# Kernel optimization log

Hardware: AMD Instinct MI355X
Metric: run time of the kernel (lower is better)

The kernel has to match this reference:

```python
import jax, jax.numpy as jnp
import numpy as np

B, L, HID = 2, 2048, 1024
H = 16
D = HID // H          # head_dim = 64
LR = 16               # gate low-rank dim
EPS = 1e-5
GLN = 16.0            # gate_logit_normalizer
SCALE = D ** -0.5


def setup_inputs() -> dict:
    key = jax.random.key(0)
    ks = jax.random.split(key, 9)
    s = 0.02
    return {
        "x": jax.random.normal(ks[0], (B, L, HID), jnp.float32),
        "Wq": jax.random.normal(ks[1], (HID, HID), jnp.float32) * s,
        "Wk": jax.random.normal(ks[2], (HID, HID), jnp.float32) * s,
        "Wv": jax.random.normal(ks[3], (HID, HID), jnp.float32) * s,
        "Wg1": jax.random.normal(ks[4], (HID, LR), jnp.float32) * s,
        "Wg2": jax.random.normal(ks[5], (LR, HID), jnp.float32) * s,
        "bg2": jnp.zeros((HID,), jnp.float32),
        "Wg": jax.random.normal(ks[6], (HID, HID), jnp.float32) * s,
        "g_norm_w": jnp.ones((D,), jnp.float32),
        "Wo": jax.random.normal(ks[7], (HID, HID), jnp.float32) * s,
    }


def reference(x, Wq, Wk, Wv, Wg1, Wg2, bg2, Wg, g_norm_w, Wo):
    Bb, Ll, Hid = x.shape
    q = (x @ Wq).reshape(Bb, Ll, H, D)
    k = (x @ Wk).reshape(Bb, Ll, H, D)
    v = (x @ Wv).reshape(Bb, Ll, H, D)
    gk = jax.nn.log_sigmoid(((x @ Wg1) @ Wg2 + bg2)).reshape(Bb, Ll, H, D) / GLN

    def step(S, inp):
        q_t, k_t, v_t, gk_t = inp  # each (B, H, D)
        # S: (B,H,D,D); gate broadcasts over the v-dim (last axis)
        S = jnp.exp(gk_t)[..., None] * S + k_t[..., None] * v_t[..., None, :]
        o_t = jnp.einsum('bhdv,bhd->bhv', S, q_t) * SCALE  # S^T @ q / sqrt(D)
        return S, o_t

    S0 = jnp.zeros((Bb, H, D, D), x.dtype)
    scan_in = tuple(jnp.moveaxis(t, 1, 0) for t in (q, k, v, gk))  # (L,B,H,D)
    S, o = jax.lax.scan(step, S0, scan_in)
    o = jnp.moveaxis(o, 0, 1)  # (B, L, H, D)

    # RMSNorm over head_dim with affine weight
    o = o * jax.lax.rsqrt(jnp.mean(o * o, axis=-1, keepdims=True) + EPS) * g_norm_w
    o = o.reshape(Bb, Ll, Hid)

    # Swish output gate
    g = x @ Wg
    o = o * (g * jax.nn.sigmoid(g))
    o = o @ Wo
    return o, S[:, None]  # last_state: (B,1,H,D,D)
```

## Files before the change

### kernel.cpp

```cpp
#include <hip/hip_runtime.h>
#include <hip/hip_bf16.h>

typedef unsigned short u16;
typedef __attribute__((ext_vector_type(8))) short bf16x8;
typedef __attribute__((ext_vector_type(4))) float f32x4;

#define L_SEQ 2048
#define HID 1024
#define NC 32
#define MTOK 4096
#define GEPS 1e-5f
#define QSCALE 0.125f

__device__ __forceinline__ float bf2f(u16 u){ union{unsigned i; float f;}c; c.i=(unsigned)u<<16; return c.f; }
__device__ __forceinline__ u16 f2bf(float f){ union{__hip_bfloat16 h; u16 u;}c; c.h=__float2bfloat16(f); return c.u; }

__device__ __forceinline__ int swz72(int row, int col){ return row * 72 + (col ^ ((row >> 1) & 24)); }
__device__ __forceinline__ int swzc(int t){ return ((t >> 2) & 3) << 3; }

__device__ __forceinline__ void gload_lds16(const u16* g, u16* l){
  __builtin_amdgcn_global_load_lds((const __attribute__((address_space(1))) void*)g,
                                   (__attribute__((address_space(3))) void*)l, 16, 0, 0);
}

__global__ __launch_bounds__(256) void gla_prep(const float* __restrict__ x,
                                                u16* __restrict__ xb,
                                                const float* W0, const float* W1,
                                                const float* W2, const float* W3,
                                                const float* W4,
                                                u16* D0, u16* D1, u16* D2, u16* D3, u16* D4){
  __shared__ float tile[32][33];
  int bid = blockIdx.x;
  if (bid < 2048){
    size_t i = ((size_t)bid * 256 + threadIdx.x) * 8;
    float4 a = *(const float4*)&x[i];
    float4 b = *(const float4*)&x[i + 4];
    u16 o[8] __attribute__((aligned(16))) = {
      f2bf(a.x), f2bf(a.y), f2bf(a.z), f2bf(a.w),
      f2bf(b.x), f2bf(b.y), f2bf(b.z), f2bf(b.w) };
    *(uint4*)&xb[i] = *(uint4*)o;
  } else {
    int id = bid - 2048;
    int z = id >> 10, rem = id & 1023;
    int bx = rem & 31, by = rem >> 5;
    const float* W; u16* D;
    switch (z){
      case 0: W = W0; D = D0; break;
      case 1: W = W1; D = D1; break;
      case 2: W = W2; D = D2; break;
      case 3: W = W3; D = D3; break;
      default: W = W4; D = D4; break;
    }
    int tx = threadIdx.x & 31, ty = threadIdx.x >> 5;
    int n0 = bx * 32, k0 = by * 32;
    #pragma unroll
    for (int r = ty; r < 32; r += 8)
      tile[r][tx] = W[(size_t)(k0 + r) * HID + n0 + tx];
    __syncthreads();
    #pragma unroll
    for (int r = ty; r < 32; r += 8)
      D[(size_t)(n0 + r) * HID + k0 + tx] = f2bf(tile[tx][r]);
  }
}

__global__ __launch_bounds__(256) void gla_xg1_mfma(const u16* __restrict__ xb,
                                                    const float* __restrict__ Wg1,
                                                    float* __restrict__ xg1){
  __shared__ u16 WL[16 * 1032];
  #pragma unroll 8
  for (int i = 0; i < 64; i++){
    int flat = i * 256 + threadIdx.x;
    int k = flat >> 4, n = flat & 15;
    WL[n * 1032 + k] = f2bf(Wg1[flat]);
  }
  __syncthreads();
  int lane = threadIdx.x & 63, w = threadIdx.x >> 6;
  int lr = lane & 15, lk = lane >> 4;
  int rt = blockIdx.x * 4 + w;
  const u16* Arow = xb + ((size_t)rt * 16 + lr) * HID;
  f32x4 acc;
  #pragma unroll
  for (int e = 0; e < 4; e++) acc[e] = 0.f;
  #pragma unroll 4
  for (int ks = 0; ks < 32; ks++){
    bf16x8 a = *(const bf16x8*)&Arow[ks * 32 + lk * 8];
    bf16x8 b = *(const bf16x8*)&WL[lr * 1032 + ks * 32 + lk * 8];
    acc = __builtin_amdgcn_mfma_f32_16x16x32_bf16(a, b, acc, 0, 0, 0);
  }
  #pragma unroll
  for (int r = 0; r < 4; r++)
    xg1[(size_t)(rt * 16 + lk * 4 + r) * 16 + lr] = acc[r];
}

__global__ __launch_bounds__(256) void gla_gkcg(const float* __restrict__ xg1,
                                                const float* __restrict__ Wg2,
                                                const float* __restrict__ bg2,
                                                u16* __restrict__ CG){
  __shared__ float xs[64][16];
  int blk = blockIdx.x;
  int b = blk >> 7, r7 = blk & 127;
  int c = r7 >> 2, q = r7 & 3;
  int col = q * 256 + threadIdx.x;
  int tok0 = b * L_SEQ + c * 64;
  {
    int row = threadIdx.x >> 2, e4 = (threadIdx.x & 3) * 4;
    *(float4*)&xs[row][e4] = *(const float4*)&xg1[(size_t)(tok0 + row) * 16 + e4];
  }
  __syncthreads();
  float w[16];
  #pragma unroll
  for (int r = 0; r < 16; r++) w[r] = Wg2[r * HID + col];
  float bz = bg2[col];
  float cum = 0.f;
  for (int t = 0; t < 64; t++){
    float z = bz;
    #pragma unroll
    for (int r = 0; r < 16; r++) z += xs[t][r] * w[r];
    float ls = -__logf(1.f + __expf(-z));
    cum += ls * (1.0f / 16.0f);
    CG[(size_t)(tok0 + t) * HID + col] = f2bf(cum);
  }
}

__global__ __launch_bounds__(512) void gla_gemm_qkvg(const u16* __restrict__ A,
                                                     const u16* __restrict__ Bt,
                                                     u16* __restrict__ C){
  constexpr int NT = HID / 32;
  __shared__ u16 As[2][256 * 32];
  __shared__ u16 Bs[2][128 * 32];
  const int tid = threadIdx.x;
  const int lane = tid & 63, wid = tid >> 6;
  const int wm = wid >> 1, wn = wid & 1;
  const int lr = lane & 15, lk = lane >> 4;
  const int id = blockIdx.x + 16 * blockIdx.y;
  const int nid = (id & 7) * 64 + (id >> 3);
  const int bm = nid & 15, bn = nid >> 4;
  const int srow = tid >> 2;
  const int skw  = ((tid & 3) * 8) ^ ((srow & 3) << 3);
  const u16* Ag = A  + ((size_t)bm * 256 + srow) * HID + skw;
  const u16* Bg = Bt + ((size_t)bn * 128 + srow) * HID + skw;

  f32x4 acc[4][4];
  #pragma unroll
  for (int i = 0; i < 4; i++)
    #pragma unroll
    for (int j = 0; j < 4; j++)
      #pragma unroll
      for (int e = 0; e < 4; e++) acc[i][j][e] = 0.f;

  auto STAGE = [&](int buf, int kt){
    gload_lds16(Ag + kt * 32,                         &As[buf][tid * 8]);
    gload_lds16(Ag + (size_t)128 * HID + kt * 32,     &As[buf][4096 + tid * 8]);
    gload_lds16(Bg + kt * 32,                         &Bs[buf][tid * 8]);
  };

  STAGE(0, 0);
  for (int t = 0; t < NT; ++t){
    const int buf = t & 1;
    if (t + 1 < NT){
      STAGE(buf ^ 1, t + 1);
      asm volatile("s_waitcnt vmcnt(3)\ns_barrier" ::: "memory");
    } else {
      asm volatile("s_waitcnt vmcnt(0)\ns_barrier" ::: "memory");
    }
    bf16x8 af[4], bfr[4];
    #pragma unroll
    for (int m = 0; m < 4; m++){
      int row = wm * 64 + m * 16 + lr;
      af[m] = *(const bf16x8*)&As[buf][(row * 32 + lk * 8) ^ ((row & 3) << 3)];
    }
    #pragma unroll
    for (int n = 0; n < 4; n++){
      int row = wn * 64 + n * 16 + lr;
      bfr[n] = *(const bf16x8*)&Bs[buf][(row * 32 + lk * 8) ^ ((row & 3) << 3)];
    }
    __builtin_amdgcn_s_setprio(1);
    #pragma unroll
    for (int m = 0; m < 4; m++)
      #pragma unroll
      for (int n = 0; n < 4; n++)
        acc[m][n] = __builtin_amdgcn_mfma_f32_16x16x32_bf16(af[m], bfr[n], acc[m][n], 0, 0, 0);
    __builtin_amdgcn_s_setprio(0);
    __builtin_amdgcn_sched_barrier(0);
    asm volatile("s_barrier" ::: "memory");
  }

  #pragma unroll
  for (int i = 0; i < 4; i++)
    #pragma unroll
    for (int j = 0; j < 4; j++){
      int row0 = bm * 256 + wm * 64 + i * 16 + lk * 4;
      int cb   = bn * 128 + wn * 64 + j * 16 + lr;
      int sel  = cb >> 10, col = cb & 1023;
      size_t base = (size_t)sel * ((size_t)MTOK * HID) + (size_t)row0 * HID + col;
      #pragma unroll
      for (int r = 0; r < 4; r++)
        C[base + (size_t)r * HID] = f2bf(acc[i][j][r]);
    }
}

__global__ __launch_bounds__(256) void gla_gemm_out2(const u16* __restrict__ A,
                                                     const u16* __restrict__ Bt,
                                                     float* __restrict__ C){
  constexpr int NT = 16;
  __shared__ __align__(16) char smem[49152];
  const int tid = threadIdx.x;
  const int lane = tid & 63, wid = tid >> 6;
  const int kg = wid >> 1, w = wid & 1;
  const int lr = lane & 15, lk = lane >> 4;
  const int bm = blockIdx.x, bn = blockIdx.y;
  const int srow = tid >> 2;
  const int skw  = ((tid & 3) * 8) ^ ((srow & 3) << 3);
  const u16* Ag = A  + ((size_t)bm * 64  + srow) * HID + skw;
  const u16* Bg = Bt + ((size_t)bn * 128 + srow) * HID + skw;
  auto seg = [&](int g, int buf) -> u16* { return (u16*)(smem + (g * 2 + buf) * 12288); };

  f32x4 acc[4][4];
  #pragma unroll
  for (int i = 0; i < 4; i++)
    #pragma unroll
    for (int j = 0; j < 4; j++)
      #pragma unroll
      for (int e = 0; e < 4; e++) acc[i][j][e] = 0.f;

  auto STAGE = [&](int buf, int kt){
    gload_lds16(Ag + kt * 32,                          seg(0, buf) + tid * 8);
    gload_lds16(Bg + kt * 32,                          seg(0, buf) + 2048 + tid * 8);
    gload_lds16(Bg + (size_t)64 * HID + kt * 32,       seg(0, buf) + 4096 + tid * 8);
    gload_lds16(Ag + 512 + kt * 32,                    seg(1, buf) + tid * 8);
    gload_lds16(Bg + 512 + kt * 32,                    seg(1, buf) + 2048 + tid * 8);
    gload_lds16(Bg + (size_t)64 * HID + 512 + kt * 32, seg(1, buf) + 4096 + tid * 8);
  };

  STAGE(0, 0);
  for (int t = 0; t < NT; ++t){
    const int buf = t & 1;
    if (t + 1 < NT){
      STAGE(buf ^ 1, t + 1);
      asm volatile("s_waitcnt vmcnt(6)\ns_barrier" ::: "memory");
    } else {
      asm volatile("s_waitcnt vmcnt(0)\ns_barrier" ::: "memory");
    }
    const u16* Ab = seg(kg, buf);
    const u16* Bb = seg(kg, buf) + 2048;
    bf16x8 af[4], bfr[4];
    #pragma unroll
    for (int m = 0; m < 4; m++){
      int row = m * 16 + lr;
      af[m] = *(const bf16x8*)&Ab[(row * 32 + lk * 8) ^ ((row & 3) << 3)];
    }
    #pragma unroll
    for (int n = 0; n < 4; n++){
      int row = w * 64 + n * 16 + lr;
      bfr[n] = *(const bf16x8*)&Bb[(row * 32 + lk * 8) ^ ((row & 3) << 3)];
    }
    __builtin_amdgcn_s_setprio(1);
    #pragma unroll
    for (int m = 0; m < 4; m++)
      #pragma unroll
      for (int n = 0; n < 4; n++)
        acc[m][n] = __builtin_amdgcn_mfma_f32_16x16x32_bf16(af[m], bfr[n], acc[m][n], 0, 0, 0);
    __builtin_amdgcn_s_setprio(0);
    __builtin_amdgcn_sched_barrier(0);
    asm volatile("s_barrier" ::: "memory");
  }

  float* red = (float*)smem;
  if (kg == 1){
    #pragma unroll
    for (int m = 0; m < 4; m++)
      #pragma unroll
      for (int n = 0; n < 4; n++){
        int lrow = m * 16 + lk * 4, lcol = w * 64 + n * 16 + lr;
        #pragma unroll
        for (int r = 0; r < 4; r++)
          red[(lrow + r) * 132 + lcol] = acc[m][n][r];
      }
  }
  __syncthreads();
  if (kg == 0){
    #pragma unroll
    for (int m = 0; m < 4; m++)
      #pragma unroll
      for (int n = 0; n < 4; n++){
        int lrow = m * 16 + lk * 4, lcol = w * 64 + n * 16 + lr;
        #pragma unroll
        for (int r = 0; r < 4; r++)
          C[(size_t)(bm * 64 + lrow + r) * HID + bn * 128 + lcol] =
              acc[m][n][r] + red[(lrow + r) * 132 + lcol];
      }
  }
}

__global__ __launch_bounds__(256) void gla_chunk_state2(const u16* __restrict__ Kb,
                                                        const u16* __restrict__ Vb,
                                                        const u16* __restrict__ CG,
                                                        u16* __restrict__ Tbuf,
                                                        float* __restrict__ Dbuf){
  __shared__ u16 KHT[64 * 72];
  __shared__ u16 VT[64 * 72];
  int blk = blockIdx.x;
  int c = blk & (NC - 1), bh = blk >> 5;
  int b = bh >> 4, h = bh & 15;
  int tid = threadIdx.x;
  int lane = tid & 63, w = tid >> 6;
  int lr = lane & 15, lk = lane >> 4;
  int tr = tid >> 2, tc = (tid & 3) * 16;
  size_t gbase = ((size_t)(b * L_SEQ + c * 64)) * HID + h * 64;

  float cg[16], cgl[16];
  {
    const u16* cgp = CG + gbase + (size_t)tr * HID + tc;
    const u16* clp = CG + gbase + (size_t)63 * HID + tc;
    uint4 a0 = *(const uint4*)cgp, a1 = *(const uint4*)(cgp + 8);
    uint4 l0 = *(const uint4*)clp, l1 = *(const uint4*)(clp + 8);
    const u16* au = (const u16*)&a0; const u16* au2 = (const u16*)&a1;
    const u16* lu = (const u16*)&l0; const u16* lu2 = (const u16*)&l1;
    #pragma unroll
    for (int e = 0; e < 8; e++){
      cg[e] = bf2f(au[e]); cg[8 + e] = bf2f(au2[e]);
      cgl[e] = bf2f(lu[e]); cgl[8 + e] = bf2f(lu2[e]);
    }
  }
  {
    const u16* kp = Kb + gbase + (size_t)tr * HID + tc;
    const u16* vp = Vb + gbase + (size_t)tr * HID + tc;
    uint4 kr0 = *(const uint4*)kp, kr1 = *(const uint4*)(kp + 8);
    uint4 vr0 = *(const uint4*)vp, vr1 = *(const uint4*)(vp + 8);
    const u16* ku = (const u16*)&kr0; const u16* ku2 = (const u16*)&kr1;
    const u16* vu = (const u16*)&vr0; const u16* vu2 = (const u16*)&vr1;
    #pragma unroll
    for (int e = 0; e < 8; e++){
      KHT[swz72(tc + e, tr)]     = f2bf(bf2f(ku[e])  * __expf(cgl[e]     - cg[e]));
      KHT[swz72(tc + 8 + e, tr)] = f2bf(bf2f(ku2[e]) * __expf(cgl[8 + e] - cg[8 + e]));
      VT[swz72(tc + e, tr)]      = vu[e];
      VT[swz72(tc + 8 + e, tr)]  = vu2[e];
    }
  }
  if (tr == 0){
    #pragma unroll
    for (int e = 0; e < 16; e++)
      Dbuf[(size_t)blk * 64 + tc + e] = __expf(cgl[e]);
  }
  __syncthreads();
  int R0 = w * 16;
  f32x4 tacc[4];
  #pragma unroll
  for (int v = 0; v < 4; v++)
    #pragma unroll
    for (int e = 0; e < 4; e++) tacc[v][e] = 0.f;
  #pragma unroll
  for (int ks = 0; ks < 2; ks++){
    bf16x8 a = *(const bf16x8*)&KHT[swz72(R0 + lr, ks * 32 + lk * 8)];
    #pragma unroll
    for (int v0 = 0; v0 < 4; v0++){
      bf16x8 bb = *(const bf16x8*)&VT[swz72(v0 * 16 + lr, ks * 32 + lk * 8)];
      tacc[v0] = __builtin_amdgcn_mfma_f32_16x16x32_bf16(a, bb, tacc[v0], 0, 0, 0);
    }
  }
  u16* Tp = Tbuf + (size_t)blk * 4096;
  #pragma unroll
  for (int v0 = 0; v0 < 4; v0++){
    int d = R0 + lk * 4, v = v0 * 16 + lr;
    #pragma unroll
    for (int r = 0; r < 4; r++)
      Tp[(d + r) * 64 + v] = f2bf(tacc[v0][r]);
  }
}

__global__ __launch_bounds__(256) void gla_state_scan2(const u16* __restrict__ Tbuf,
                                                       const float* __restrict__ Dbuf,
                                                       float* __restrict__ Sfin,
                                                       u16* __restrict__ Sinb){
  int bh = blockIdx.x >> 4, seg = blockIdx.x & 15;
  int dv = seg * 256 + threadIdx.x;
  int d = dv >> 6;
  float S = 0.f;
  for (int c = 0; c < NC; c++){
    size_t slot = (size_t)bh * NC + c;
    float t  = bf2f(Tbuf[slot * 4096 + dv]);
    float dec = Dbuf[slot * 64 + d];
    Sinb[slot * 4096 + dv] = f2bf(S);
    S = dec * S + t;
  }
  Sfin[(size_t)bh * 4096 + dv] = S;
}

__global__ __launch_bounds__(256) void gla_chunk_out2(const u16* __restrict__ Qb,
                                                      const u16* __restrict__ Kb,
                                                      const u16* __restrict__ Vb,
                                                      const u16* __restrict__ CG,
                                                      const u16* __restrict__ Sinb,
                                                      const u16* __restrict__ Gb,
                                                      const float* __restrict__ gnw,
                                                      u16* __restrict__ OG){
  __shared__ u16 QT[64 * 72];
  __shared__ u16 KP[64 * 72];
  __shared__ u16 VT[64 * 72];
  __shared__ u16 ST[64 * 72];
  int blk = blockIdx.x;
  int c = blk & (NC - 1), bh = blk >> 5;
  int b = bh >> 4, h = bh & 15;
  int tid = threadIdx.x;
  int lane = tid & 63, w = tid >> 6;
  int lr = lane & 15, lk = lane >> 4;
  int tr = tid >> 2, tc = (tid & 3) * 16;
  size_t gbase = ((size_t)(b * L_SEQ + c * 64)) * HID + h * 64;

  {
    float cg[16];
    const u16* cgp = CG + gbase + (size_t)tr * HID + tc;
    uint4 a0 = *(const uint4*)cgp, a1 = *(const uint4*)(cgp + 8);
    const u16* au = (const u16*)&a0; const u16* au2 = (const u16*)&a1;
    #pragma unroll
    for (int e = 0; e < 8; e++){ cg[e] = bf2f(au[e]); cg[8 + e] = bf2f(au2[e]); }
    const u16* qp = Qb + gbase + (size_t)tr * HID + tc;
    const u16* kp = Kb + gbase + (size_t)tr * HID + tc;
    const u16* vp = Vb + gbase + (size_t)tr * HID + tc;
    uint4 qr0 = *(const uint4*)qp, qr1 = *(const uint4*)(qp + 8);
    uint4 kr0 = *(const uint4*)kp, kr1 = *(const uint4*)(kp + 8);
    uint4 vr0 = *(const uint4*)vp, vr1 = *(const uint4*)(vp + 8);
    const u16* qu = (const u16*)&qr0; const u16* qu2 = (const u16*)&qr1;
    const u16* ku = (const u16*)&kr0; const u16* ku2 = (const u16*)&kr1;
    const u16* vu = (const u16*)&vr0; const u16* vu2 = (const u16*)&vr1;
    u16 qt[16] __attribute__((aligned(16)));
    u16 kt[16] __attribute__((aligned(16)));
    #pragma unroll
    for (int e = 0; e < 8; e++){
      float ec0 = __expf(cg[e]),  ei0 = __expf(-cg[e]);
      float ec1 = __expf(cg[8+e]), ei1 = __expf(-cg[8+e]);
      qt[e]     = f2bf(bf2f(qu[e])  * ec0 * QSCALE);
      qt[8 + e] = f2bf(bf2f(qu2[e]) * ec1 * QSCALE);
      kt[e]     = f2bf(bf2f(ku[e])  * ei0);
      kt[8 + e] = f2bf(bf2f(ku2[e]) * ei1);
      VT[swz72(tc + e, tr)]     = vu[e];
      VT[swz72(tc + 8 + e, tr)] = vu2[e];
    }
    *(uint4*)&QT[tr * 72 + tc]     = *(uint4*)&qt[0];
    *(uint4*)&QT[tr * 72 + tc + 8] = *(uint4*)&qt[8];
    *(uint4*)&KP[tr * 72 + tc]     = *(uint4*)&kt[0];
    *(uint4*)&KP[tr * 72 + tc + 8] = *(uint4*)&kt[8];
    const u16* sp = Sinb + (size_t)blk * 4096 + (size_t)tr * 64 + tc;
    uint4 s0 = *(const uint4*)sp, s1 = *(const uint4*)(sp + 8);
    const u16* su = (const u16*)&s0; const u16* su2 = (const u16*)&s1;
    #pragma unroll
    for (int e = 0; e < 8; e++){
      ST[swz72(tc + e, tr)]     = su[e];
      ST[swz72(tc + 8 + e, tr)] = su2[e];
    }
  }
  __syncthreads();

  int R0 = w * 16;
  f32x4 pacc[4];
  #pragma unroll
  for (int j = 0; j < 4; j++)
    #pragma unroll
    for (int e = 0; e < 4; e++) pacc[j][e] = 0.f;
  #pragma unroll
  for (int ks = 0; ks < 2; ks++){
    bf16x8 a = *(const bf16x8*)&QT[(R0 + lr) * 72 + ks * 32 + lk * 8];
    #pragma unroll
    for (int j0 = 0; j0 < 4; j0++){
      bf16x8 bb = *(const bf16x8*)&KP[(j0 * 16 + lr) * 72 + ks * 32 + lk * 8];
      pacc[j0] = __builtin_amdgcn_mfma_f32_16x16x32_bf16(a, bb, pacc[j0], 0, 0, 0);
    }
  }
  __syncthreads();

  #pragma unroll
  for (int j0 = 0; j0 < 4; j0++){
    int j = j0 * 16 + lr;
    #pragma unroll
    for (int r = 0; r < 4; r++){
      int t = R0 + lk * 4 + r;
      KP[t * 72 + (j ^ swzc(t))] = (j <= t) ? f2bf(pacc[j0][r]) : (u16)0;
    }
  }

  f32x4 oacc[4];
  #pragma unroll
  for (int v = 0; v < 4; v++)
    #pragma unroll
    for (int e = 0; e < 4; e++) oacc[v][e] = 0.f;
  #pragma unroll
  for (int ks = 0; ks < 2; ks++){
    bf16x8 a = *(const bf16x8*)&QT[(R0 + lr) * 72 + ks * 32 + lk * 8];
    #pragma unroll
    for (int v0 = 0; v0 < 4; v0++){
      bf16x8 bb = *(const bf16x8*)&ST[swz72(v0 * 16 + lr, ks * 32 + lk * 8)];
      oacc[v0] = __builtin_amdgcn_mfma_f32_16x16x32_bf16(a, bb, oacc[v0], 0, 0, 0);
    }
  }
  #pragma unroll
  for (int ks = 0; ks < 2; ks++){
    int arow = R0 + lr;
    bf16x8 a = *(const bf16x8*)&KP[arow * 72 + ((ks * 32 + lk * 8) ^ swzc(arow))];
    #pragma unroll
    for (int v0 = 0; v0 < 4; v0++){
      bf16x8 bb = *(const bf16x8*)&VT[swz72(v0 * 16 + lr, ks * 32 + lk * 8)];
      oacc[v0] = __builtin_amdgcn_mfma_f32_16x16x32_bf16(a, bb, oacc[v0], 0, 0, 0);
    }
  }

  {
    float gv[4][4];
    #pragma unroll
    for (int r = 0; r < 4; r++){
      int t = R0 + lk * 4 + r;
      #pragma unroll
      for (int v0 = 0; v0 < 4; v0++)
        gv[r][v0] = bf2f(Gb[gbase + (size_t)t * HID + v0 * 16 + lr]);
    }
    float gnv[4];
    #pragma unroll
    for (int v0 = 0; v0 < 4; v0++) gnv[v0] = gnw[v0 * 16 + lr];
    #pragma unroll
    for (int r = 0; r < 4; r++){
      float ssq = 0.f;
      #pragma unroll
      for (int v0 = 0; v0 < 4; v0++) ssq += oacc[v0][r] * oacc[v0][r];
      ssq += __shfl_xor(ssq, 1, 64);
      ssq += __shfl_xor(ssq, 2, 64);
      ssq += __shfl_xor(ssq, 4, 64);
      ssq += __shfl_xor(ssq, 8, 64);
      float rn = rsqrtf(ssq * (1.0f / 64.0f) + GEPS);
      int t = R0 + lk * 4 + r;
      #pragma unroll
      for (int v0 = 0; v0 < 4; v0++){
        float g = gv[r][v0];
        float sw = g / (1.f + __expf(-g));
        QT[t * 72 + ((v0 * 16 + lr) ^ swzc(t))] = f2bf(oacc[v0][r] * rn * gnv[v0] * sw);
      }
    }
  }
  __syncthreads();
  {
    int x0 = swzc(tr);
    uint4 o0 = *(uint4*)&QT[tr * 72 + (tc ^ x0)];
    uint4 o1 = *(uint4*)&QT[tr * 72 + ((tc + 8) ^ x0)];
    u16* op = OG + gbase + (size_t)tr * HID + tc;
    *(uint4*)op       = o0;
    *(uint4*)(op + 8) = o1;
  }
}

extern "C" void kernel_launch(void* const* d_in, const int* in_sizes, int n_in,
                              void* d_out, int out_size, void* d_ws, size_t ws_size,
                              hipStream_t stream){
  (void)in_sizes; (void)n_in; (void)out_size;
  const float* x   = (const float*)d_in[0];
  const float* Wq  = (const float*)d_in[1];
  const float* Wk  = (const float*)d_in[2];
  const float* Wv  = (const float*)d_in[3];
  const float* Wg1 = (const float*)d_in[4];
  const float* Wg2 = (const float*)d_in[5];
  const float* bg2 = (const float*)d_in[6];
  const float* Wg  = (const float*)d_in[7];
  const float* gnw = (const float*)d_in[8];
  const float* Wo  = (const float*)d_in[9];
  float* out = (float*)d_out;

  char* ws = (char*)d_ws;
  size_t off = 0;
  auto alloc = [&](size_t bytes) -> char* {
    char* p = ws + off; off += (bytes + 255) & ~(size_t)255; return p;
  };
  u16* xb   = (u16*)alloc((size_t)MTOK * HID * 2);
  u16* WTq  = (u16*)alloc((size_t)HID * HID * 2);
  u16* WTk  = (u16*)alloc((size_t)HID * HID * 2);
  u16* WTv  = (u16*)alloc((size_t)HID * HID * 2);
  u16* WTg  = (u16*)alloc((size_t)HID * HID * 2);
  u16* WTo  = (u16*)alloc((size_t)HID * HID * 2);
  u16* Qb   = (u16*)alloc((size_t)MTOK * HID * 2);
  u16* Kb   = (u16*)alloc((size_t)MTOK * HID * 2);
  u16* Vb   = (u16*)alloc((size_t)MTOK * HID * 2);
  u16* Gb   = (u16*)alloc((size_t)MTOK * HID * 2);
  u16* CGb  = (u16*)alloc((size_t)MTOK * HID * 2);
  float* xg1b = (float*)alloc((size_t)MTOK * 16 * 4);
  u16* Tbuf = (u16*)alloc((size_t)1024 * 4096 * 2);
  float* Dbuf = (float*)alloc((size_t)1024 * 64 * 4);
  u16* Sinb = (u16*)alloc((size_t)1024 * 4096 * 2);
  u16* OG   = (u16*)alloc((size_t)MTOK * HID * 2);
  if (off > ws_size) return;

  gla_prep<<<7168, 256, 0, stream>>>(x, xb, Wq, Wk, Wv, Wg, Wo,
                                     WTq, WTk, WTv, WTg, WTo);
  gla_xg1_mfma<<<64, 256, 0, stream>>>(xb, Wg1, xg1b);
  gla_gkcg<<<256, 256, 0, stream>>>(xg1b, Wg2, bg2, CGb);

  dim3 gq(16, 32);
  gla_gemm_qkvg<<<gq, 512, 0, stream>>>(xb, WTq, Qb);

  gla_chunk_state2<<<1024, 256, 0, stream>>>(Kb, Vb, CGb, Tbuf, Dbuf);
  gla_state_scan2<<<512, 256, 0, stream>>>(Tbuf, Dbuf, out + (size_t)MTOK * HID, Sinb);
  gla_chunk_out2<<<1024, 256, 0, stream>>>(Qb, Kb, Vb, CGb, Sinb, Gb, gnw, OG);

  dim3 go(64, 8);
  gla_gemm_out2<<<go, 256, 0, stream>>>(OG, WTo, out);
}
```

Measured before the change: 118.6 us.

## Fold gate low-rank GEMM into prep, parallelize gate cumsum, vectorize state scan

The x@Wg1 MFMA kernel is merged into the prep kernel as extra blocks that read fp32 x directly and convert it to bf16 on the fly, which removes one launch. The gate cumsum kernel is rewritten to use 1024 blocks, each covering a 64-token by 64-column tile. The sigmoid values go through shared memory and a two-level prefix sum replaces the serial 64-step loop per thread. The state scan now handles two elements per thread with packed 32-bit loads and stores, using half as many blocks. Together these target launch overhead and the low parallelism of the serial gate scan, at the cost of more shared memory per block and more synchronization.

```diff
diff --git a/kernel.cpp b/kernel.cpp
--- a/kernel.cpp
+++ b/kernel.cpp
@@ -25,11 +25,13 @@
 
 __global__ __launch_bounds__(256) void gla_prep(const float* __restrict__ x,
                                                 u16* __restrict__ xb,
+                                                const float* __restrict__ Wg1,
+                                                float* __restrict__ xg1,
                                                 const float* W0, const float* W1,
                                                 const float* W2, const float* W3,
                                                 const float* W4,
                                                 u16* D0, u16* D1, u16* D2, u16* D3, u16* D4){
-  __shared__ float tile[32][33];
+  __shared__ union { float tile[32][33]; u16 WL[16 * 1032]; } sh;
   int bid = blockIdx.x;
   if (bid < 2048){
     size_t i = ((size_t)bid * 256 + threadIdx.x) * 8;
@@ -39,7 +41,7 @@
       f2bf(a.x), f2bf(a.y), f2bf(a.z), f2bf(a.w),
       f2bf(b.x), f2bf(b.y), f2bf(b.z), f2bf(b.w) };
     *(uint4*)&xb[i] = *(uint4*)o;
-  } else {
+  } else if (bid < 7168){
     int id = bid - 2048;
     int z = id >> 10, rem = id & 1023;
     int bx = rem & 31, by = rem >> 5;
@@ -55,71 +57,92 @@
     int n0 = bx * 32, k0 = by * 32;
     #pragma unroll
     for (int r = ty; r < 32; r += 8)
-      tile[r][tx] = W[(size_t)(k0 + r) * HID + n0 + tx];
+      sh.tile[r][tx] = W[(size_t)(k0 + r) * HID + n0 + tx];
     __syncthreads();
     #pragma unroll
     for (int r = ty; r < 32; r += 8)
-      D[(size_t)(n0 + r) * HID + k0 + tx] = f2bf(tile[tx][r]);
-  }
-}
-
-__global__ __launch_bounds__(256) void gla_xg1_mfma(const u16* __restrict__ xb,
-                                                    const float* __restrict__ Wg1,
-                                                    float* __restrict__ xg1){
-  __shared__ u16 WL[16 * 1032];
-  #pragma unroll 8
-  for (int i = 0; i < 64; i++){
-    int flat = i * 256 + threadIdx.x;
-    int k = flat >> 4, n = flat & 15;
-    WL[n * 1032 + k] = f2bf(Wg1[flat]);
-  }
-  __syncthreads();
-  int lane = threadIdx.x & 63, w = threadIdx.x >> 6;
-  int lr = lane & 15, lk = lane >> 4;
-  int rt = blockIdx.x * 4 + w;
-  const u16* Arow = xb + ((size_t)rt * 16 + lr) * HID;
-  f32x4 acc;
-  #pragma unroll
-  for (int e = 0; e < 4; e++) acc[e] = 0.f;
-  #pragma unroll 4
-  for (int ks = 0; ks < 32; ks++){
-    bf16x8 a = *(const bf16x8*)&Arow[ks * 32 + lk * 8];
-    bf16x8 b = *(const bf16x8*)&WL[lr * 1032 + ks * 32 + lk * 8];
-    acc = __builtin_amdgcn_mfma_f32_16x16x32_bf16(a, b, acc, 0, 0, 0);
-  }
-  #pragma unroll
-  for (int r = 0; r < 4; r++)
-    xg1[(size_t)(rt * 16 + lk * 4 + r) * 16 + lr] = acc[r];
-}
-
-__global__ __launch_bounds__(256) void gla_gkcg(const float* __restrict__ xg1,
-                                                const float* __restrict__ Wg2,
-                                                const float* __restrict__ bg2,
-                                                u16* __restrict__ CG){
-  __shared__ float xs[64][16];
+      D[(size_t)(n0 + r) * HID + k0 + tx] = f2bf(sh.tile[tx][r]);
+  } else {
+    #pragma unroll 8
+    for (int i = 0; i < 64; i++){
+      int flat = i * 256 + threadIdx.x;
+      int k = flat >> 4, n = flat & 15;
+      sh.WL[n * 1032 + k] = f2bf(Wg1[flat]);
+    }
+    __syncthreads();
+    int lane = threadIdx.x & 63, w = threadIdx.x >> 6;
+    int lr = lane & 15, lk = lane >> 4;
+    int rt = (bid - 7168) * 4 + w;
+    const float* Arow = x + ((size_t)rt * 16 + lr) * HID;
+    f32x4 acc;
+    #pragma unroll
+    for (int e = 0; e < 4; e++) acc[e] = 0.f;
+    #pragma unroll 4
+    for (int ks = 0; ks < 32; ks++){
+      float4 a0 = *(const float4*)&Arow[ks * 32 + lk * 8];
+      float4 a1 = *(const float4*)&Arow[ks * 32 + lk * 8 + 4];
+      u16 av[8] __attribute__((aligned(16))) = {
+        f2bf(a0.x), f2bf(a0.y), f2bf(a0.z), f2bf(a0.w),
+        f2bf(a1.x), f2bf(a1.y), f2bf(a1.z), f2bf(a1.w) };
+      bf16x8 a = *(bf16x8*)av;
+      bf16x8 b = *(const bf16x8*)&sh.WL[lr * 1032 + ks * 32 + lk * 8];
+      acc = __builtin_amdgcn_mfma_f32_16x16x32_bf16(a, b, acc, 0, 0, 0);
+    }
+    #pragma unroll
+    for (int r = 0; r < 4; r++)
+      xg1[(size_t)(rt * 16 + lk * 4 + r) * 16 + lr] = acc[r];
+  }
+}
+
+__global__ __launch_bounds__(256) void gla_gkcg2(const float* __restrict__ xg1,
+                                                 const float* __restrict__ Wg2,
+                                                 const float* __restrict__ bg2,
+                                                 u16* __restrict__ CG){
+  __shared__ float xs[64][17];
+  __shared__ float wg[16][64];
+  __shared__ float lss[64][65];
+  __shared__ float red[4][64];
   int blk = blockIdx.x;
-  int b = blk >> 7, r7 = blk & 127;
-  int c = r7 >> 2, q = r7 & 3;
-  int col = q * 256 + threadIdx.x;
+  int bc = blk >> 4, cgi = blk & 15;
+  int b = bc >> 5, c = bc & 31;
+  int col0 = cgi * 64;
   int tok0 = b * L_SEQ + c * 64;
+  int tid = threadIdx.x;
   {
-    int row = threadIdx.x >> 2, e4 = (threadIdx.x & 3) * 4;
-    *(float4*)&xs[row][e4] = *(const float4*)&xg1[(size_t)(tok0 + row) * 16 + e4];
-  }
-  __syncthreads();
-  float w[16];
-  #pragma unroll
-  for (int r = 0; r < 16; r++) w[r] = Wg2[r * HID + col];
-  float bz = bg2[col];
-  float cum = 0.f;
-  for (int t = 0; t < 64; t++){
-    float z = bz;
-    #pragma unroll
-    for (int r = 0; r < 16; r++) z += xs[t][r] * w[r];
-    float ls = -__logf(1.f + __expf(-z));
-    cum += ls * (1.0f / 16.0f);
-    CG[(size_t)(tok0 + t) * HID + col] = f2bf(cum);
-  }
+    int row = tid >> 2, e4 = (tid & 3) * 4;
+    float4 v = *(const float4*)&xg1[(size_t)(tok0 + row) * 16 + e4];
+    xs[row][e4 + 0] = v.x; xs[row][e4 + 1] = v.y;
+    xs[row][e4 + 2] = v.z; xs[row][e4 + 3] = v.w;
+    int f = tid * 4; int r = f >> 6, cc = f & 63;
+    *(float4*)&wg[r][cc] = *(const float4*)&Wg2[(size_t)r * HID + col0 + cc];
+  }
+  __syncthreads();
+  int t = tid & 63, cq = tid >> 6;
+  float xr[16];
+  #pragma unroll
+  for (int r = 0; r < 16; r++) xr[r] = xs[t][r];
+  #pragma unroll
+  for (int i = 0; i < 16; i++){
+    int col = cq * 16 + i;
+    float z = bg2[col0 + col];
+    #pragma unroll
+    for (int r = 0; r < 16; r++) z += xr[r] * wg[r][col];
+    lss[t][col] = -__logf(1.f + __expf(-z)) * (1.0f / 16.0f);
+  }
+  __syncthreads();
+  int col = tid & 63, q = tid >> 6;
+  float cum16[16];
+  float s = 0.f;
+  #pragma unroll
+  for (int i = 0; i < 16; i++){ s += lss[q * 16 + i][col]; cum16[i] = s; }
+  red[q][col] = s;
+  __syncthreads();
+  float offs = 0.f;
+  #pragma unroll
+  for (int p = 0; p < 3; p++) if (p < q) offs += red[p][col];
+  #pragma unroll
+  for (int i = 0; i < 16; i++)
+    CG[(size_t)(tok0 + q * 16 + i) * HID + col0 + col] = f2bf(offs + cum16[i]);
 }
 
 __global__ __launch_bounds__(512) void gla_gemm_qkvg(const u16* __restrict__ A,
@@ -368,22 +391,25 @@
   }
 }
 
-__global__ __launch_bounds__(256) void gla_state_scan2(const u16* __restrict__ Tbuf,
+__global__ __launch_bounds__(256) void gla_state_scan3(const u16* __restrict__ Tbuf,
                                                        const float* __restrict__ Dbuf,
                                                        float* __restrict__ Sfin,
                                                        u16* __restrict__ Sinb){
-  int bh = blockIdx.x >> 4, seg = blockIdx.x & 15;
-  int dv = seg * 256 + threadIdx.x;
+  int bh = blockIdx.x >> 3, seg = blockIdx.x & 7;
+  int dv = seg * 512 + threadIdx.x * 2;
   int d = dv >> 6;
-  float S = 0.f;
+  float S0 = 0.f, S1 = 0.f;
   for (int c = 0; c < NC; c++){
     size_t slot = (size_t)bh * NC + c;
-    float t  = bf2f(Tbuf[slot * 4096 + dv]);
+    unsigned tv = *(const unsigned*)&Tbuf[slot * 4096 + dv];
     float dec = Dbuf[slot * 64 + d];
-    Sinb[slot * 4096 + dv] = f2bf(S);
-    S = dec * S + t;
-  }
-  Sfin[(size_t)bh * 4096 + dv] = S;
+    unsigned sv = (unsigned)f2bf(S0) | ((unsigned)f2bf(S1) << 16);
+    *(unsigned*)&Sinb[slot * 4096 + dv] = sv;
+    S0 = dec * S0 + bf2f((u16)(tv & 0xffff));
+    S1 = dec * S1 + bf2f((u16)(tv >> 16));
+  }
+  float2 sf = make_float2(S0, S1);
+  *(float2*)&Sfin[(size_t)bh * 4096 + dv] = sf;
 }
 
 __global__ __launch_bounds__(256) void gla_chunk_out2(const u16* __restrict__ Qb,
@@ -584,16 +610,15 @@
   u16* OG   = (u16*)alloc((size_t)MTOK * HID * 2);
   if (off > ws_size) return;
 
-  gla_prep<<<7168, 256, 0, stream>>>(x, xb, Wq, Wk, Wv, Wg, Wo,
+  gla_prep<<<7232, 256, 0, stream>>>(x, xb, Wg1, xg1b, Wq, Wk, Wv, Wg, Wo,
                                      WTq, WTk, WTv, WTg, WTo);
-  gla_xg1_mfma<<<64, 256, 0, stream>>>(xb, Wg1, xg1b);
-  gla_gkcg<<<256, 256, 0, stream>>>(xg1b, Wg2, bg2, CGb);
+  gla_gkcg2<<<1024, 256, 0, stream>>>(xg1b, Wg2, bg2, CGb);
 
   dim3 gq(16, 32);
   gla_gemm_qkvg<<<gq, 512, 0, stream>>>(xb, WTq, Qb);
 
   gla_chunk_state2<<<1024, 256, 0, stream>>>(Kb, Vb, CGb, Tbuf, Dbuf);
-  gla_state_scan2<<<512, 256, 0, stream>>>(Tbuf, Dbuf, out + (size_t)MTOK * HID, Sinb);
+  gla_state_scan3<<<256, 256, 0, stream>>>(Tbuf, Dbuf, out + (size_t)MTOK * HID, Sinb);
   gla_chunk_out2<<<1024, 256, 0, stream>>>(Qb, Kb, Vb, CGb, Sinb, Gb, gnw, OG);
 
   dim3 go(64, 8);
```

After: 126.1 us. 6.3% more time.
